# Kernel tuning notes

Measured on AMD Instinct MI355X. Metric: run time of the kernel, lower is better.

## Reference

```python
import jax, jax.numpy as jnp
import numpy as np
import math

N_HEADS = 16
D_MODEL = 1024
D_FF = 4096
MAX_REL = 32  # max_relative_position
LN_EPS = 1e-5


def _layernorm(x, g, b):
    m = jnp.mean(x, axis=-1, keepdims=True)
    v = jnp.var(x, axis=-1, keepdims=True)
    return (x - m) * jax.lax.rsqrt(v + LN_EPS) * g + b


def setup_inputs() -> dict:
    key = jax.random.key(0)
    ks = jax.random.split(key, 12)
    D, F = D_MODEL, D_FF
    gain = 1.0 / math.sqrt(2.0)
    xav = lambda k, o, i, g=1.0: jax.random.uniform(k, (o, i), jnp.float32, -1.0, 1.0) * (g * math.sqrt(6.0 / (o + i)))
    return {
        "x": jax.random.normal(ks[0], (2, 2048, D), jnp.float32),
        "wq": xav(ks[1], D, D, gain),
        "wk": xav(ks[2], D, D, gain),
        "wv": xav(ks[3], D, D, gain),
        "wo": xav(ks[4], D, D, gain),
        "wo_b": jnp.zeros((D,), jnp.float32),
        "rel_tab": jax.random.normal(ks[5], (2 * MAX_REL - 1, N_HEADS), jnp.float32) * 0.02,
        "ln1_g": jnp.ones((D,), jnp.float32),
        "ln1_b": jnp.zeros((D,), jnp.float32),
        "ln2_g": jnp.ones((D,), jnp.float32),
        "ln2_b": jnp.zeros((D,), jnp.float32),
        "w1": xav(ks[6], F, D),
        "b1": jnp.zeros((F,), jnp.float32),
        "w2": xav(ks[7], D, F),
        "b2": jnp.zeros((D,), jnp.float32),
    }


def reference(x, wq, wk, wv, wo, wo_b, rel_tab, ln1_g, ln1_b, ln2_g, ln2_b, w1, b1, w2, b2):
    B, S, D = x.shape
    H = N_HEADS
    dk = D // H

    def proj(w):  # torch Linear: x @ w.T, then split heads -> [B,H,S,dk]
        return (x @ w.T).reshape(B, S, H, dk).transpose(0, 2, 1, 3)

    q, k, v = proj(wq), proj(wk), proj(wv)

    # Rotary embeddings (per-head dim), exact interleave-to-block formula from source
    t = jnp.arange(S, dtype=jnp.float32)
    inv_freq = 1.0 / (10000.0 ** (jnp.arange(0, dk, 2, dtype=jnp.float32) / dk))
    freqs = t[:, None] * inv_freq[None, :]  # [S, dk/2]
    cos, sin = jnp.cos(freqs), jnp.sin(freqs)

    def rope(z):
        z1, z2 = z[..., ::2], z[..., 1::2]  # [B,H,S,dk/2]
        return jnp.concatenate([z1 * cos - z2 * sin, z1 * sin + z2 * cos], axis=-1)

    q, k = rope(q), rope(k)

    # Manual attention with learned relative-position bias
    scores = jnp.einsum("bhqd,bhkd->bhqk", q, k) / math.sqrt(dk)
    rel = jnp.arange(S)[:, None] - jnp.arange(S)[None, :]
    rel = jnp.clip(rel, -(MAX_REL - 1), MAX_REL - 1) + (MAX_REL - 1)
    bias = rel_tab[rel]  # [S,S,H]
    scores = scores + jnp.transpose(bias, (2, 0, 1))[None]  # [1,H,S,S]
    attn = jax.nn.softmax(scores, axis=-1)
    o = jnp.einsum("bhqk,bhkd->bhqd", attn, v).transpose(0, 2, 1, 3).reshape(B, S, D)
    o = o @ wo.T + wo_b

    # Post-norm residual block
    h = _layernorm(x + o, ln1_g, ln1_b)
    f = jax.nn.gelu(h @ w1.T + b1, approximate=False) @ w2.T + b2
    return _layernorm(h + f, ln2_g, ln2_b)
```

## Files before the change

kernel.cpp:

```cpp
#include <hip/hip_runtime.h>
#include <stdint.h>

#define MB (1ull << 20)
typedef unsigned short u16;
typedef __attribute__((ext_vector_type(8))) short bf16x8;
typedef __attribute__((ext_vector_type(4))) float f32x4;

__device__ __forceinline__ float b2f(u16 u) {
  union { unsigned int i; float f; } c; c.i = ((unsigned int)u) << 16; return c.f;
}
__device__ __forceinline__ u16 f2b(float f) {
  union { float f; unsigned int i; } c; c.f = f;
  unsigned int r = c.i + 0x7fffu + ((c.i >> 16) & 1u);
  return (u16)(r >> 16);
}
__device__ __forceinline__ void gload16(const void* g, void* l) {
  __builtin_amdgcn_global_load_lds(
      (const __attribute__((address_space(1))) void*)g,
      (__attribute__((address_space(3))) void*)l, 16, 0, 0);
}

__global__ __launch_bounds__(256) void f2b_all(
    const float* __restrict__ x, const float* __restrict__ wq, const float* __restrict__ wk,
    const float* __restrict__ wv, const float* __restrict__ wo, const float* __restrict__ w1,
    const float* __restrict__ w2,
    u16* __restrict__ xb, u16* __restrict__ wqkvb, u16* __restrict__ wob,
    u16* __restrict__ w1b, u16* __restrict__ w2b)
{
  int bid = blockIdx.x;
  const float* src; u16* dst;
  if (bid < 4096)       { src = x;  dst = xb; }
  else if (bid < 5120)  { src = wq; dst = wqkvb;           bid -= 4096; }
  else if (bid < 6144)  { src = wk; dst = wqkvb + 1048576; bid -= 5120; }
  else if (bid < 7168)  { src = wv; dst = wqkvb + 2097152; bid -= 6144; }
  else if (bid < 8192)  { src = wo; dst = wob;             bid -= 7168; }
  else if (bid < 12288) { src = w1; dst = w1b;             bid -= 8192; }
  else                  { src = w2; dst = w2b;             bid -= 12288; }
  int i = (bid * 256 + threadIdx.x) * 4;
  float4 v = *(const float4*)(src + i);
  uint2 ov;
  ov.x = (unsigned)f2b(v.x) | ((unsigned)f2b(v.y) << 16);
  ov.y = (unsigned)f2b(v.z) | ((unsigned)f2b(v.w) << 16);
  *(uint2*)(dst + i) = ov;
}

__global__ __launch_bounds__(256) void rope_tab_kernel(float2* __restrict__ tab) {
  int idx = blockIdx.x * 256 + threadIdx.x;
  int s = idx >> 5, j = idx & 31;
  float inv = exp2f(-(float)j * (13.287712379549449f / 32.0f));
  float sn, cs;
  sincosf((float)s * inv, &sn, &cs);
  tab[idx] = make_float2(cs, sn);
}

__global__ __launch_bounds__(256) void gemm_ks(
    const u16* __restrict__ A, const u16* __restrict__ B,
    u16* __restrict__ C, int M, int N, int K)
{
  constexpr int BM = 64, MT = 2;
  __shared__ __align__(16) u16 As[BM * 64];
  __shared__ __align__(16) u16 Bs[128 * 64];
  const int tid = threadIdx.x;
  const int lane = tid & 63, wave = tid >> 6;
  const int lr = lane & 15, lg = lane >> 4;
  const int wm = wave >> 1, wn = wave & 1;

  const int nwg = gridDim.x * gridDim.y;
  const int id = blockIdx.y * gridDim.x + blockIdx.x;
  const int nid = (id & 7) * (nwg >> 3) + (id >> 3);
  const int bx = nid % gridDim.x, byk = nid / gridDim.x;
  const int kslice = byk & 1, by = byk >> 1;
  const int Kh = K >> 1;
  const int kofs = kslice * Kh;
  u16* Cs = C + (size_t)kslice * M * N;

  const int srow = tid >> 3;
  const int scsw = ((tid & 7) * 8) ^ ((srow & 7) << 3);
  const size_t abase = (size_t)(by * BM + srow) * K + kofs + scsw;
  const size_t bbase = (size_t)(bx * 128 + srow) * K + kofs + scsw;

  int aoff[MT][2], boff[4][2];
  #pragma unroll
  for (int mt = 0; mt < MT; mt++) {
    int row = wm * (BM / 2) + mt * 16 + lr;
    #pragma unroll
    for (int kk = 0; kk < 2; kk++)
      aoff[mt][kk] = row * 64 + ((kk * 32 + lg * 8) ^ ((row & 7) << 3));
  }
  #pragma unroll
  for (int nt = 0; nt < 4; nt++) {
    int row = wn * 64 + nt * 16 + lr;
    #pragma unroll
    for (int kk = 0; kk < 2; kk++)
      boff[nt][kk] = row * 64 + ((kk * 32 + lg * 8) ^ ((row & 7) << 3));
  }

  f32x4 acc[MT][4];
  #pragma unroll
  for (int i = 0; i < MT; i++)
    #pragma unroll
    for (int j = 0; j < 4; j++) acc[i][j] = (f32x4){0.f, 0.f, 0.f, 0.f};

  for (int k0 = 0; k0 < Kh; k0 += 64) {
    __syncthreads();
    #pragma unroll
    for (int h = 0; h < MT; h++)
      gload16(A + abase + (size_t)(h * 32) * K + k0, &As[h * 2048 + tid * 8]);
    #pragma unroll
    for (int h = 0; h < 4; h++)
      gload16(B + bbase + (size_t)(h * 32) * K + k0, &Bs[h * 2048 + tid * 8]);
    __syncthreads();
    #pragma unroll
    for (int kk = 0; kk < 2; kk++) {
      bf16x8 af[MT], bfr[4];
      #pragma unroll
      for (int mt = 0; mt < MT; mt++) af[mt] = *(const bf16x8*)&As[aoff[mt][kk]];
      #pragma unroll
      for (int nt = 0; nt < 4; nt++) bfr[nt] = *(const bf16x8*)&Bs[boff[nt][kk]];
      #pragma unroll
      for (int mt = 0; mt < MT; mt++)
        #pragma unroll
        for (int nt = 0; nt < 4; nt++)
          acc[mt][nt] = __builtin_amdgcn_mfma_f32_16x16x32_bf16(af[mt], bfr[nt], acc[mt][nt], 0, 0, 0);
    }
  }

  #pragma unroll
  for (int mt = 0; mt < MT; mt++)
    #pragma unroll
    for (int nt = 0; nt < 4; nt++) {
      const int row = by * BM + wm * (BM / 2) + mt * 16 + lg * 4;
      const int col = bx * 128 + wn * 64 + nt * 16 + lr;
      #pragma unroll
      for (int r = 0; r < 4; r++)
        Cs[(size_t)(row + r) * N + col] = f2b(acc[mt][nt][r]);
    }
}

#define MFMA16(BASE, BF)                                                       \
  __builtin_amdgcn_s_setprio(1);                                               \
  _Pragma("unroll")                                                            \
  for (int mt = 0; mt < 4; mt++)                                               \
    _Pragma("unroll")                                                          \
    for (int nt = 0; nt < 4; nt++)                                             \
      acc[(BASE) + mt][nt] = __builtin_amdgcn_mfma_f32_16x16x32_bf16(          \
          af[mt], BF[nt], acc[(BASE) + mt][nt], 0, 0, 0);                      \
  __builtin_amdgcn_s_setprio(0);

#define SA2(bb, eta, kb)                                                             \
  gload16(Ab + ((size_t)(eta) * 128) * K + (kb), &As[bb][eta][tid * 8]);             \
  gload16(Ab + ((size_t)(eta) * 128 + 64) * K + (kb), &As[bb][eta][4096 + tid * 8]);
#define SB2(bb, eta, kb)                                                             \
  gload16(Bb + ((size_t)(eta) * 128) * K + (kb), &Bs[bb][eta][tid * 8]);             \
  gload16(Bb + ((size_t)(eta) * 128 + 64) * K + (kb), &Bs[bb][eta][4096 + tid * 8]);

#define SBAR asm volatile("s_barrier" ::: "memory")

template<int EPI>
__global__ __launch_bounds__(512) void gemm256(
    const u16* __restrict__ A, const u16* __restrict__ B,
    u16* __restrict__ C, const float* __restrict__ bias,
    int M, int N, int K)
{
  __shared__ __align__(16) u16 As[2][2][8192];
  __shared__ __align__(16) u16 Bs[2][2][8192];
  const int tid = threadIdx.x;
  const int lane = tid & 63, wave = tid >> 6;
  const int lr = lane & 15, lg = lane >> 4;
  const int wm = wave >> 2, wn = wave & 3;

  const int nwg = gridDim.x * gridDim.y;
  const int id = blockIdx.y * gridDim.x + blockIdx.x;
  const int nid = (id & 7) * (nwg >> 3) + (id >> 3);
  const int bx = nid % gridDim.x, by = nid / gridDim.x;

  const int srow = tid >> 3;
  const int scsw = ((tid & 7) * 8) ^ ((srow & 7) << 3);
  const u16* Ab = A + (size_t)(by * 256 + srow) * K + scsw;
  const u16* Bb = B + (size_t)(bx * 256 + srow) * K + scsw;

  int aoff[2][2][4], boff[2][4];
  #pragma unroll
  for (int mh = 0; mh < 2; mh++)
    #pragma unroll
    for (int kk = 0; kk < 2; kk++)
      #pragma unroll
      for (int mt = 0; mt < 4; mt++) {
        int row = mh * 64 + mt * 16 + lr;
        aoff[mh][kk][mt] = row * 64 + ((kk * 32 + lg * 8) ^ ((lr & 7) << 3));
      }
  #pragma unroll
  for (int kk = 0; kk < 2; kk++)
    #pragma unroll
    for (int nt = 0; nt < 4; nt++) {
      int row = (wn & 1) * 64 + nt * 16 + lr;
      boff[kk][nt] = row * 64 + ((kk * 32 + lg * 8) ^ ((lr & 7) << 3));
    }

  f32x4 acc[8][4];
  #pragma unroll
  for (int i = 0; i < 8; i++)
    #pragma unroll
    for (int j = 0; j < 4; j++) acc[i][j] = (f32x4){0.f, 0.f, 0.f, 0.f};

  const int NT = K >> 6;

  SB2(0, 0, 0) SB2(0, 1, 0) SA2(0, 0, 0) SA2(0, 1, 0)

  for (int t = 0; t < NT; ++t) {
    const int c = t & 1, n = c ^ 1;
    const size_t kb = (size_t)(t + 1) * 64;
    const bool st = (t + 1 < NT);
    const u16* Ac = As[c][wm];
    const u16* Bc = Bs[c][wn >> 1];
    bf16x8 b0[4], b1[4], af[4];

    asm volatile("s_waitcnt vmcnt(0)" ::: "memory");
    SBAR;
    #pragma unroll
    for (int nt = 0; nt < 4; nt++) b0[nt] = *(const bf16x8*)&Bc[boff[0][nt]];
    #pragma unroll
    for (int mt = 0; mt < 4; mt++) af[mt] = *(const bf16x8*)&Ac[aoff[0][0][mt]];
    if (st) { SB2(n, 0, kb) }
    MFMA16(0, b0)
    SBAR;
    #pragma unroll
    for (int nt = 0; nt < 4; nt++) b1[nt] = *(const bf16x8*)&Bc[boff[1][nt]];
    #pragma unroll
    for (int mt = 0; mt < 4; mt++) af[mt] = *(const bf16x8*)&Ac[aoff[0][1][mt]];
    if (st) { SA2(n, 0, kb) }
    SBAR;
    MFMA16(0, b1)
    SBAR;
    #pragma unroll
    for (int mt = 0; mt < 4; mt++) af[mt] = *(const bf16x8*)&Ac[aoff[1][0][mt]];
    if (st) { SB2(n, 1, kb) }
    SBAR;
    MFMA16(4, b0)
    SBAR;
    #pragma unroll
    for (int mt = 0; mt < 4; mt++) af[mt] = *(const bf16x8*)&Ac[aoff[1][1][mt]];
    if (st) { SA2(n, 1, kb) }
    SBAR;
    MFMA16(4, b1)
    SBAR;
  }

  #pragma unroll
  for (int m8 = 0; m8 < 8; m8++)
    #pragma unroll
    for (int nt = 0; nt < 4; nt++) {
      const int row = by * 256 + wm * 128 + m8 * 16 + lg * 4;
      const int col = bx * 256 + wn * 64 + nt * 16 + lr;
      const float bv = (EPI >= 1) ? bias[col] : 0.f;
      #pragma unroll
      for (int r = 0; r < 4; r++) {
        float x = acc[m8][nt][r] + bv;
        if (EPI == 2) x = 0.5f * x * (1.f + erff(x * 0.70710678118654752f));
        C[(size_t)(row + r) * N + col] = f2b(x);
      }
    }
}

__global__ __launch_bounds__(256) void rope_kernel(
    const u16* __restrict__ qp, const u16* __restrict__ kp, int stride,
    const float2* __restrict__ tab, u16* __restrict__ qr, u16* __restrict__ kr)
{
  const int gid = blockIdx.x * 4 + (threadIdx.x >> 6);
  const int lane = threadIdx.x & 63;
  const int s = gid & 2047;
  const int bh = gid >> 11;
  const int h = bh & 15, b = bh >> 4;
  const int j = lane & 31;
  float2 t = tab[s * 32 + j];
  const float cs = t.x, sn = t.y;
  const size_t base = (size_t)(b * 2048 + s) * stride + h * 64;
  unsigned int qv = *(const unsigned int*)(qp + base + 2 * j);
  unsigned int kv = *(const unsigned int*)(kp + base + 2 * j);
  float q1 = b2f((u16)qv), q2 = b2f((u16)(qv >> 16));
  float k1 = b2f((u16)kv), k2 = b2f((u16)(kv >> 16));
  float qo = (lane < 32) ? (q1 * cs - q2 * sn) : (q1 * sn + q2 * cs);
  float ko = (lane < 32) ? (k1 * cs - k2 * sn) : (k1 * sn + k2 * cs);
  qr[(size_t)gid * 64 + lane] = f2b(qo * 0.18033688011112042f);
  kr[(size_t)gid * 64 + lane] = f2b(ko);
}

__global__ __launch_bounds__(256) void vtrans_kernel(
    const u16* __restrict__ vp, int stride, u16* __restrict__ vT)
{
  __shared__ u16 t[64][65];
  const int sc = blockIdx.x & 31;
  const int bh = blockIdx.x >> 5;
  const int h = bh & 15, b = bh >> 4;
  const int tid = threadIdx.x;
  #pragma unroll
  for (int i = 0; i < 16; i++) {
    int idx = i * 256 + tid;
    int sl = idx >> 6, d = idx & 63;
    t[sl][d] = vp[(size_t)(b * 2048 + sc * 64 + sl) * stride + h * 64 + d];
  }
  __syncthreads();
  #pragma unroll
  for (int i = 0; i < 16; i++) {
    int idx = i * 256 + tid;
    int d = idx >> 6, sl = idx & 63;
    vT[((size_t)bh * 64 + d) * 2048 + sc * 64 + sl] = t[sl][d];
  }
}

__global__ __launch_bounds__(256) void attn_kernel(
    const u16* __restrict__ qr, const u16* __restrict__ kr,
    const u16* __restrict__ vT, const float* __restrict__ rel_tab,
    u16* __restrict__ o)
{
  __shared__ __align__(16) u16 Ks[2][64 * 64];
  __shared__ __align__(16) u16 Vs[2][64 * 64];
  __shared__ float bias_s[64];

  const int tid = threadIdx.x;
  const int lane = tid & 63, wave = tid >> 6;
  const int lr = lane & 15, lg = lane >> 4;

  const int id = blockIdx.x;
  const int nid = (id & 7) * 128 + (id >> 3);
  const int bh = nid >> 5, qc = nid & 31;
  const int h = bh & 15, b = bh >> 4;
  const int q0 = qc * 64 + wave * 16;

  if (tid < 63) bias_s[tid] = rel_tab[tid * 16 + h] * 1.4426950408889634f;

  const u16* qb = qr + (size_t)bh * 2048 * 64;
  const u16* kb = kr + (size_t)bh * 2048 * 64;
  const u16* vb = vT + (size_t)bh * 64 * 2048;

  bf16x8 qf[2];
  qf[0] = *(const bf16x8*)(qb + (size_t)(q0 + lr) * 64 + lg * 8);
  qf[1] = *(const bf16x8*)(qb + (size_t)(q0 + lr) * 64 + 32 + lg * 8);

  const int srow = tid >> 3;
  const int scsw = ((tid & 7) * 8) ^ ((srow & 7) << 3);

  int koff[4][2];
  #pragma unroll
  for (int nt = 0; nt < 4; nt++)
    #pragma unroll
    for (int ks = 0; ks < 2; ks++)
      koff[nt][ks] = (nt * 16 + lr) * 64 + ((ks * 32 + lg * 8) ^ ((lr & 7) << 3));

  #pragma unroll
  for (int hh = 0; hh < 2; hh++) {
    gload16(kb + (size_t)(hh * 32 + srow) * 64 + scsw, &Ks[0][hh * 2048 + tid * 8]);
    gload16(vb + (size_t)(hh * 32 + srow) * 2048 + scsw, &Vs[0][hh * 2048 + tid * 8]);
  }

  float mrow = -1e30f;
  f32x4 lvec = (f32x4){0.f, 0.f, 0.f, 0.f};
  f32x4 oacc[4];
  #pragma unroll
  for (int nt = 0; nt < 4; nt++) oacc[nt] = (f32x4){0.f, 0.f, 0.f, 0.f};

  const int idx_lo = 4 * (lr + 16 * ((lg & 1) * 2));
  const int idx_hi = idx_lo + 64;
  const bool hiSel = (lg >= 2);

  int cur = 0;
  for (int kc = 0; kc < 32; kc++) {
    const int k0 = kc * 64;
    __syncthreads();
    if (kc < 31) {
      const int kn = k0 + 64;
      #pragma unroll
      for (int hh = 0; hh < 2; hh++) {
        gload16(kb + (size_t)(kn + hh * 32 + srow) * 64 + scsw, &Ks[cur ^ 1][hh * 2048 + tid * 8]);
        gload16(vb + (size_t)(hh * 32 + srow) * 2048 + kn + scsw, &Vs[cur ^ 1][hh * 2048 + tid * 8]);
      }
    }
    const u16* Kc = Ks[cur];
    const u16* Vc = Vs[cur];

    f32x4 sacc[4];
    #pragma unroll
    for (int nt = 0; nt < 4; nt++) sacc[nt] = (f32x4){0.f, 0.f, 0.f, 0.f};
    __builtin_amdgcn_s_setprio(1);
    #pragma unroll
    for (int ks = 0; ks < 2; ks++)
      #pragma unroll
      for (int nt = 0; nt < 4; nt++) {
        bf16x8 kf = *(const bf16x8*)&Kc[koff[nt][ks]];
        sacc[nt] = __builtin_amdgcn_mfma_f32_16x16x32_bf16(kf, qf[ks], sacc[nt], 0, 0, 0);
      }
    __builtin_amdgcn_s_setprio(0);

    f32x4 pvv[4];
    const int dmin = q0 - k0 - 63, dmax = q0 + 15 - k0;
    if (dmin >= 31 || dmax <= -31) {
      const float c = bias_s[dmin >= 31 ? 62 : 0];
      f32x4 m4;
      #pragma unroll
      for (int i = 0; i < 4; i++)
        m4[i] = fmaxf(fmaxf(sacc[0][i], sacc[1][i]), fmaxf(sacc[2][i], sacc[3][i]));
      float rm = fmaxf(fmaxf(m4[0], m4[1]), fmaxf(m4[2], m4[3])) + c;
      rm = fmaxf(rm, __shfl_xor(rm, 16));
      rm = fmaxf(rm, __shfl_xor(rm, 32));
      if (!__all(rm <= mrow + 11.5f)) {
        float mnew = fmaxf(mrow, rm);
        float sc = exp2f(mrow - mnew);
        lvec *= sc;
        #pragma unroll
        for (int nt = 0; nt < 4; nt++) oacc[nt] *= sc;
        mrow = mnew;
      }
      const float off = c - mrow;
      #pragma unroll
      for (int nt = 0; nt < 4; nt++) pvv[nt] = sacc[nt] + off;
    } else {
      #pragma unroll
      for (int nt = 0; nt < 4; nt++)
        #pragma unroll
        for (int r = 0; r < 4; r++) {
          int d = (q0 + lr) - (k0 + nt * 16 + lg * 4 + r);
          d = d < -31 ? -31 : (d > 31 ? 31 : d);
          pvv[nt][r] = sacc[nt][r] + bias_s[d + 31];
        }
      f32x4 m4;
      #pragma unroll
      for (int i = 0; i < 4; i++)
        m4[i] = fmaxf(fmaxf(pvv[0][i], pvv[1][i]), fmaxf(pvv[2][i], pvv[3][i]));
      float rm = fmaxf(fmaxf(m4[0], m4[1]), fmaxf(m4[2], m4[3]));
      rm = fmaxf(rm, __shfl_xor(rm, 16));
      rm = fmaxf(rm, __shfl_xor(rm, 32));
      if (!__all(rm <= mrow + 11.5f)) {
        float mnew = fmaxf(mrow, rm);
        float sc = exp2f(mrow - mnew);
        lvec *= sc;
        #pragma unroll
        for (int nt = 0; nt < 4; nt++) oacc[nt] *= sc;
        mrow = mnew;
      }
      #pragma unroll
      for (int nt = 0; nt < 4; nt++) pvv[nt] = pvv[nt] - mrow;
    }

    unsigned int pk[4][2];
    #pragma unroll
    for (int nt = 0; nt < 4; nt++) {
      f32x4 p;
      #pragma unroll
      for (int i = 0; i < 4; i++) p[i] = exp2f(pvv[nt][i]);
      lvec += p;
      unsigned int pr0, pr1;
      asm("v_cvt_pk_bf16_f32 %0, %1, %2" : "=v"(pr0) : "v"(p[0]), "v"(p[1]));
      asm("v_cvt_pk_bf16_f32 %0, %1, %2" : "=v"(pr1) : "v"(p[2]), "v"(p[3]));
      pk[nt][0] = pr0;
      pk[nt][1] = pr1;
    }

    __builtin_amdgcn_s_setprio(1);
    #pragma unroll
    for (int ks = 0; ks < 2; ks++) {
      int w0a = __builtin_amdgcn_ds_bpermute(idx_lo, (int)pk[ks * 2][0]);
      int w0b = __builtin_amdgcn_ds_bpermute(idx_lo, (int)pk[ks * 2 + 1][0]);
      int w1a = __builtin_amdgcn_ds_bpermute(idx_lo, (int)pk[ks * 2][1]);
      int w1b = __builtin_amdgcn_ds_bpermute(idx_lo, (int)pk[ks * 2 + 1][1]);
      int w2a = __builtin_amdgcn_ds_bpermute(idx_hi, (int)pk[ks * 2][0]);
      int w2b = __builtin_amdgcn_ds_bpermute(idx_hi, (int)pk[ks * 2 + 1][0]);
      int w3a = __builtin_amdgcn_ds_bpermute(idx_hi, (int)pk[ks * 2][1]);
      int w3b = __builtin_amdgcn_ds_bpermute(idx_hi, (int)pk[ks * 2 + 1][1]);
      int4 bw;
      bw.x = hiSel ? w0b : w0a;
      bw.y = hiSel ? w1b : w1a;
      bw.z = hiSel ? w2b : w2a;
      bw.w = hiSel ? w3b : w3a;
      bf16x8 pf = *(bf16x8*)&bw;
      #pragma unroll
      for (int nt = 0; nt < 4; nt++) {
        bf16x8 vf = *(const bf16x8*)&Vc[koff[nt][ks]];
        oacc[nt] = __builtin_amdgcn_mfma_f32_16x16x32_bf16(vf, pf, oacc[nt], 0, 0, 0);
      }
    }
    __builtin_amdgcn_s_setprio(0);
    cur ^= 1;
  }

  float lpart = (lvec[0] + lvec[1]) + (lvec[2] + lvec[3]);
  lpart += __shfl_xor(lpart, 16);
  lpart += __shfl_xor(lpart, 32);
  const float inv = 1.0f / lpart;
  const size_t obase = (size_t)(b * 2048 + q0 + lr) * 1024 + h * 64;
  #pragma unroll
  for (int nt = 0; nt < 4; nt++) {
    uint2 st;
    st.x = (unsigned)f2b(oacc[nt][0] * inv) | ((unsigned)f2b(oacc[nt][1] * inv) << 16);
    st.y = (unsigned)f2b(oacc[nt][2] * inv) | ((unsigned)f2b(oacc[nt][3] * inv) << 16);
    *(uint2*)(o + obase + nt * 16 + lg * 4) = st;
  }
}

__global__ __launch_bounds__(256) void ln1_kernel(
    const float* __restrict__ x, const u16* __restrict__ ao0,
    const u16* __restrict__ ao1, const float* __restrict__ wob,
    const float* __restrict__ g, const float* __restrict__ bta,
    u16* __restrict__ hb)
{
  const int row = blockIdx.x, tid = threadIdx.x;
  const int wave = tid >> 6, lane = tid & 63;
  const int c = tid * 4;
  float4 xv = *(const float4*)(x + (size_t)row * 1024 + c);
  uint2 a0 = *(const uint2*)(ao0 + (size_t)row * 1024 + c);
  uint2 a1 = *(const uint2*)(ao1 + (size_t)row * 1024 + c);
  float4 wb = *(const float4*)(wob + c);
  float v0 = xv.x + b2f((u16)a0.x) + b2f((u16)a1.x) + wb.x;
  float v1 = xv.y + b2f((u16)(a0.x >> 16)) + b2f((u16)(a1.x >> 16)) + wb.y;
  float v2 = xv.z + b2f((u16)a0.y) + b2f((u16)a1.y) + wb.z;
  float v3 = xv.w + b2f((u16)(a0.y >> 16)) + b2f((u16)(a1.y >> 16)) + wb.w;
  float s = (v0 + v1) + (v2 + v3);
  float s2 = (v0 * v0 + v1 * v1) + (v2 * v2 + v3 * v3);
  #pragma unroll
  for (int off = 32; off >= 1; off >>= 1) { s += __shfl_down(s, off); s2 += __shfl_down(s2, off); }
  __shared__ float rs[4], rs2[4];
  if (lane == 0) { rs[wave] = s; rs2[wave] = s2; }
  __syncthreads();
  s = rs[0] + rs[1] + rs[2] + rs[3];
  s2 = rs2[0] + rs2[1] + rs2[2] + rs2[3];
  float mean = s * (1.f / 1024.f);
  float var = s2 * (1.f / 1024.f) - mean * mean;
  float inv = rsqrtf(var + 1e-5f);
  float4 gv = *(const float4*)(g + c);
  float4 bv = *(const float4*)(bta + c);
  uint2 ov;
  ov.x = (unsigned)f2b((v0 - mean) * inv * gv.x + bv.x) |
         ((unsigned)f2b((v1 - mean) * inv * gv.y + bv.y) << 16);
  ov.y = (unsigned)f2b((v2 - mean) * inv * gv.z + bv.z) |
         ((unsigned)f2b((v3 - mean) * inv * gv.w + bv.w) << 16);
  *(uint2*)(hb + (size_t)row * 1024 + c) = ov;
}

__global__ __launch_bounds__(256) void ln2_kernel(
    const u16* __restrict__ hb, const u16* __restrict__ fb0,
    const u16* __restrict__ fb1, const float* __restrict__ b2,
    const float* __restrict__ g, const float* __restrict__ bta,
    float* __restrict__ out)
{
  const int row = blockIdx.x, tid = threadIdx.x;
  const int wave = tid >> 6, lane = tid & 63;
  const int c = tid * 4;
  uint2 hv = *(const uint2*)(hb + (size_t)row * 1024 + c);
  uint2 f0 = *(const uint2*)(fb0 + (size_t)row * 1024 + c);
  uint2 f1 = *(const uint2*)(fb1 + (size_t)row * 1024 + c);
  float4 b2v = *(const float4*)(b2 + c);
  float v0 = b2f((u16)hv.x) + b2f((u16)f0.x) + b2f((u16)f1.x) + b2v.x;
  float v1 = b2f((u16)(hv.x >> 16)) + b2f((u16)(f0.x >> 16)) + b2f((u16)(f1.x >> 16)) + b2v.y;
  float v2 = b2f((u16)hv.y) + b2f((u16)f0.y) + b2f((u16)f1.y) + b2v.z;
  float v3 = b2f((u16)(hv.y >> 16)) + b2f((u16)(f0.y >> 16)) + b2f((u16)(f1.y >> 16)) + b2v.w;
  float s = (v0 + v1) + (v2 + v3);
  float s2 = (v0 * v0 + v1 * v1) + (v2 * v2 + v3 * v3);
  #pragma unroll
  for (int off = 32; off >= 1; off >>= 1) { s += __shfl_down(s, off); s2 += __shfl_down(s2, off); }
  __shared__ float rs[4], rs2[4];
  if (lane == 0) { rs[wave] = s; rs2[wave] = s2; }
  __syncthreads();
  s = rs[0] + rs[1] + rs[2] + rs[3];
  s2 = rs2[0] + rs2[1] + rs2[2] + rs2[3];
  float mean = s * (1.f / 1024.f);
  float var = s2 * (1.f / 1024.f) - mean * mean;
  float inv = rsqrtf(var + 1e-5f);
  float4 gv = *(const float4*)(g + c);
  float4 bv = *(const float4*)(bta + c);
  float4 ov;
  ov.x = (v0 - mean) * inv * gv.x + bv.x;
  ov.y = (v1 - mean) * inv * gv.y + bv.y;
  ov.z = (v2 - mean) * inv * gv.z + bv.z;
  ov.w = (v3 - mean) * inv * gv.w + bv.w;
  *(float4*)(out + (size_t)row * 1024 + c) = ov;
}

extern "C" void kernel_launch(void* const* d_in, const int* in_sizes, int n_in,
                              void* d_out, int out_size, void* d_ws, size_t ws_size,
                              hipStream_t stream)
{
  const float* x    = (const float*)d_in[0];
  const float* wq   = (const float*)d_in[1];
  const float* wk   = (const float*)d_in[2];
  const float* wv   = (const float*)d_in[3];
  const float* wo   = (const float*)d_in[4];
  const float* wo_b = (const float*)d_in[5];
  const float* rel  = (const float*)d_in[6];
  const float* ln1g = (const float*)d_in[7];
  const float* ln1b = (const float*)d_in[8];
  const float* ln2g = (const float*)d_in[9];
  const float* ln2b = (const float*)d_in[10];
  const float* w1   = (const float*)d_in[11];
  const float* b1   = (const float*)d_in[12];
  const float* w2   = (const float*)d_in[13];
  const float* b2   = (const float*)d_in[14];
  float* out = (float*)d_out;
  char* w = (char*)d_ws;

  if (ws_size < (size_t)90 * MB) return;

  u16* xb    = (u16*)(w + 0 * MB);
  u16* wqkvb = (u16*)(w + 8 * MB);
  u16* wob   = (u16*)(w + 14 * MB);
  u16* w1b   = (u16*)(w + 16 * MB);
  u16* w2b   = (u16*)(w + 24 * MB);
  u16* qkv   = (u16*)(w + 32 * MB);
  u16* ob    = (u16*)(w + 32 * MB);
  u16* ao01  = (u16*)(w + 40 * MB);
  u16* hb    = (u16*)(w + 32 * MB);
  u16* qrb   = (u16*)(w + 56 * MB);
  u16* krb   = (u16*)(w + 64 * MB);
  u16* vTb   = (u16*)(w + 72 * MB);
  u16* gb    = (u16*)(w + 56 * MB);
  u16* fb01  = (u16*)(w + 0 * MB);
  float2* tab = (float2*)(w + 88 * MB);

  const int M = 4096, D = 1024, F = 4096;

  rope_tab_kernel<<<dim3(256), 256, 0, stream>>>(tab);
  f2b_all<<<dim3(16384), 256, 0, stream>>>(x, wq, wk, wv, wo, w1, w2,
                                           xb, wqkvb, wob, w1b, w2b);

  gemm256<0><<<dim3(3 * D / 256, M / 256), 512, 0, stream>>>(xb, wqkvb, qkv, nullptr, M, 3 * D, D);

  rope_kernel<<<dim3(16384), 256, 0, stream>>>(qkv, qkv + 1024, 3 * D, tab, qrb, krb);
  vtrans_kernel<<<dim3(1024), 256, 0, stream>>>(qkv + 2048, 3 * D, vTb);

  attn_kernel<<<dim3(1024), 256, 0, stream>>>(qrb, krb, vTb, rel, ob);

  gemm_ks<<<dim3(D / 128, (M / 64) * 2), 256, 0, stream>>>(ob, wob, ao01, M, D, D);

  ln1_kernel<<<dim3(M), 256, 0, stream>>>(x, ao01, ao01 + (size_t)M * D, wo_b,
                                          ln1g, ln1b, hb);

  gemm256<2><<<dim3(F / 256, M / 256), 512, 0, stream>>>(hb, w1b, gb, b1, M, F, D);

  gemm_ks<<<dim3(D / 128, (M / 64) * 2), 256, 0, stream>>>(gb, w2b, fb01, M, D, F);

  ln2_kernel<<<dim3(M), 256, 0, stream>>>(hb, fb01, fb01 + (size_t)M * D, b2,
                                          ln2g, ln2b, out);
}
```

Baseline: 275.8 us.

## Fuse RoPE with V transpose and use permlane swaps in attention

Merges the separate RoPE and V-transpose kernels into one launch, where each block handles a 64-row sequence chunk for one head and does both the rotary update of Q/K and the transpose of V. Inside the attention kernel, the eight ds_bpermute calls plus selects that rearranged P for the PV MFMA are replaced with four v_permlane32_swap/v_permlane16_swap instructions. This removes a launch and the LDS permute traffic. It relies on the swap sequence producing the same lane layout as the old bpermute mapping.

```diff
diff --git a/kernel.cpp b/kernel.cpp
--- a/kernel.cpp
+++ b/kernel.cpp
@@ -262,43 +262,41 @@
     }
 }
 
-__global__ __launch_bounds__(256) void rope_kernel(
-    const u16* __restrict__ qp, const u16* __restrict__ kp, int stride,
-    const float2* __restrict__ tab, u16* __restrict__ qr, u16* __restrict__ kr)
-{
-  const int gid = blockIdx.x * 4 + (threadIdx.x >> 6);
-  const int lane = threadIdx.x & 63;
-  const int s = gid & 2047;
-  const int bh = gid >> 11;
-  const int h = bh & 15, b = bh >> 4;
-  const int j = lane & 31;
-  float2 t = tab[s * 32 + j];
-  const float cs = t.x, sn = t.y;
-  const size_t base = (size_t)(b * 2048 + s) * stride + h * 64;
-  unsigned int qv = *(const unsigned int*)(qp + base + 2 * j);
-  unsigned int kv = *(const unsigned int*)(kp + base + 2 * j);
-  float q1 = b2f((u16)qv), q2 = b2f((u16)(qv >> 16));
-  float k1 = b2f((u16)kv), k2 = b2f((u16)(kv >> 16));
-  float qo = (lane < 32) ? (q1 * cs - q2 * sn) : (q1 * sn + q2 * cs);
-  float ko = (lane < 32) ? (k1 * cs - k2 * sn) : (k1 * sn + k2 * cs);
-  qr[(size_t)gid * 64 + lane] = f2b(qo * 0.18033688011112042f);
-  kr[(size_t)gid * 64 + lane] = f2b(ko);
-}
-
-__global__ __launch_bounds__(256) void vtrans_kernel(
-    const u16* __restrict__ vp, int stride, u16* __restrict__ vT)
+__global__ __launch_bounds__(256) void rope_vtrans_kernel(
+    const u16* __restrict__ qkv, const float2* __restrict__ tab,
+    u16* __restrict__ qr, u16* __restrict__ kr, u16* __restrict__ vT)
 {
   __shared__ u16 t[64][65];
-  const int sc = blockIdx.x & 31;
-  const int bh = blockIdx.x >> 5;
+  const int bid = blockIdx.x;
+  const int bh = bid >> 5, sc = bid & 31;
   const int h = bh & 15, b = bh >> 4;
   const int tid = threadIdx.x;
+  const int lane = tid & 63;
+  const int j = lane & 31;
+
   #pragma unroll
   for (int i = 0; i < 16; i++) {
     int idx = i * 256 + tid;
     int sl = idx >> 6, d = idx & 63;
-    t[sl][d] = vp[(size_t)(b * 2048 + sc * 64 + sl) * stride + h * 64 + d];
-  }
+    t[sl][d] = qkv[(size_t)(b * 2048 + sc * 64 + sl) * 3072 + 2048 + h * 64 + d];
+  }
+
+  #pragma unroll
+  for (int i = 0; i < 16; i++) {
+    int s = sc * 64 + i * 4 + (tid >> 6);
+    float2 tt = tab[s * 32 + j];
+    const float cs = tt.x, sn = tt.y;
+    const size_t base = (size_t)(b * 2048 + s) * 3072 + h * 64;
+    unsigned int qv = *(const unsigned int*)(qkv + base + 2 * j);
+    unsigned int kv = *(const unsigned int*)(qkv + base + 1024 + 2 * j);
+    float q1 = b2f((u16)qv), q2 = b2f((u16)(qv >> 16));
+    float k1 = b2f((u16)kv), k2 = b2f((u16)(kv >> 16));
+    float qo = (lane < 32) ? (q1 * cs - q2 * sn) : (q1 * sn + q2 * cs);
+    float ko = (lane < 32) ? (k1 * cs - k2 * sn) : (k1 * sn + k2 * cs);
+    qr[(size_t)(bh * 2048 + s) * 64 + lane] = f2b(qo * 0.18033688011112042f);
+    kr[(size_t)(bh * 2048 + s) * 64 + lane] = f2b(ko);
+  }
+
   __syncthreads();
   #pragma unroll
   for (int i = 0; i < 16; i++) {
@@ -358,10 +356,6 @@
   f32x4 oacc[4];
   #pragma unroll
   for (int nt = 0; nt < 4; nt++) oacc[nt] = (f32x4){0.f, 0.f, 0.f, 0.f};
-
-  const int idx_lo = 4 * (lr + 16 * ((lg & 1) * 2));
-  const int idx_hi = idx_lo + 64;
-  const bool hiSel = (lg >= 2);
 
   int cur = 0;
   for (int kc = 0; kc < 32; kc++) {
@@ -458,19 +452,13 @@
     __builtin_amdgcn_s_setprio(1);
     #pragma unroll
     for (int ks = 0; ks < 2; ks++) {
-      int w0a = __builtin_amdgcn_ds_bpermute(idx_lo, (int)pk[ks * 2][0]);
-      int w0b = __builtin_amdgcn_ds_bpermute(idx_lo, (int)pk[ks * 2 + 1][0]);
-      int w1a = __builtin_amdgcn_ds_bpermute(idx_lo, (int)pk[ks * 2][1]);
-      int w1b = __builtin_amdgcn_ds_bpermute(idx_lo, (int)pk[ks * 2 + 1][1]);
-      int w2a = __builtin_amdgcn_ds_bpermute(idx_hi, (int)pk[ks * 2][0]);
-      int w2b = __builtin_amdgcn_ds_bpermute(idx_hi, (int)pk[ks * 2 + 1][0]);
-      int w3a = __builtin_amdgcn_ds_bpermute(idx_hi, (int)pk[ks * 2][1]);
-      int w3b = __builtin_amdgcn_ds_bpermute(idx_hi, (int)pk[ks * 2 + 1][1]);
-      int4 bw;
-      bw.x = hiSel ? w0b : w0a;
-      bw.y = hiSel ? w1b : w1a;
-      bw.z = hiSel ? w2b : w2a;
-      bw.w = hiSel ? w3b : w3a;
+      unsigned int r0 = pk[2 * ks][0], r1 = pk[2 * ks][1];
+      unsigned int r2 = pk[2 * ks + 1][0], r3 = pk[2 * ks + 1][1];
+      asm("v_permlane32_swap_b32 %0, %1" : "+v"(r0), "+v"(r2));
+      asm("v_permlane32_swap_b32 %0, %1" : "+v"(r1), "+v"(r3));
+      asm("v_permlane16_swap_b32 %0, %1" : "+v"(r0), "+v"(r2));
+      asm("v_permlane16_swap_b32 %0, %1" : "+v"(r1), "+v"(r3));
+      int4 bw = make_int4((int)r0, (int)r1, (int)r2, (int)r3);
       bf16x8 pf = *(bf16x8*)&bw;
       #pragma unroll
       for (int nt = 0; nt < 4; nt++) {
@@ -622,8 +610,7 @@
 
   gemm256<0><<<dim3(3 * D / 256, M / 256), 512, 0, stream>>>(xb, wqkvb, qkv, nullptr, M, 3 * D, D);
 
-  rope_kernel<<<dim3(16384), 256, 0, stream>>>(qkv, qkv + 1024, 3 * D, tab, qrb, krb);
-  vtrans_kernel<<<dim3(1024), 256, 0, stream>>>(qkv + 2048, 3 * D, vTb);
+  rope_vtrans_kernel<<<dim3(1024), 256, 0, stream>>>(qkv, tab, qrb, krb, vTb);
 
   attn_kernel<<<dim3(1024), 256, 0, stream>>>(qrb, krb, vTb, rel, ob);
 
```

After: 265.7 us. 3.6% less time.
